# Optimization experiments

Measured on AMD Instinct MI355X. Metric: run time of the kernel, lower is better.

The kernel has to match this reference:

```python
import jax, jax.numpy as jnp
import numpy as np
import math

DIM = 512

def setup_inputs() -> dict:
    key = jax.random.key(0)
    k1, k2, k3, k4 = jax.random.split(key, 4)
    B, SD, SE, D = 32, 512, 512, DIM
    padded_seqs = jax.random.normal(k1, (B, SD, D), dtype=jnp.float32)
    encoder_padded_seqs = jax.random.normal(k2, (B, SE, D), dtype=jnp.float32)
    decoder_mask = jnp.ones((B, SD, 1), dtype=jnp.float32)
    # attention linear: Linear(2*D, D) -> weight (D, 2*D), bias (D,)
    bound = 1.0 / math.sqrt(2 * D)
    W = jax.random.uniform(k3, (D, 2 * D), dtype=jnp.float32, minval=-bound, maxval=bound)
    b = jax.random.uniform(k4, (D,), dtype=jnp.float32, minval=-bound, maxval=bound)
    return {"padded_seqs": padded_seqs, "encoder_padded_seqs": encoder_padded_seqs,
            "decoder_mask": decoder_mask, "W": W, "b": b}

def reference(padded_seqs, encoder_padded_seqs, decoder_mask, W, b):
    D = padded_seqs.shape[-1]
    scale = 1.0 / math.sqrt(D)
    # scores: (B, seq_d, seq_e) via matmul instead of broadcast multiply-sum
    scores = jnp.einsum('bqd,bkd->bqk', padded_seqs, encoder_padded_seqs) * scale
    attention_weights = jax.nn.softmax(scores, axis=2)
    attention_context = jnp.einsum('bqk,bkd->bqd', attention_weights, encoder_padded_seqs)
    cat = jnp.concatenate([padded_seqs, attention_context], axis=2)  # (B, seq_d, 2D)
    attention_masked = jnp.tanh(cat @ W.T + b) * decoder_mask
    return (attention_masked, attention_weights)
```

## Files before the change

### kernel.cpp

```cpp
#include <hip/hip_runtime.h>
#include <math.h>

typedef unsigned short u16;
typedef unsigned int   u32;
typedef __attribute__((ext_vector_type(8))) short bf16x8;
typedef __attribute__((ext_vector_type(4))) float f32x4;

#define BATCH  32
#define SEQ    512
#define DM     512
#define SQE    (SEQ*DM)
#define NBE    ((size_t)BATCH*SQE)

__device__ __forceinline__ u16 f2bf(float x) {
  union { float f; u32 i; } v; v.f = x;
  u32 r = v.i + 0x7fffu + ((v.i >> 16) & 1u);
  return (u16)(r >> 16);
}
__device__ __forceinline__ float fast_tanh(float x) {
  float xc = fminf(fmaxf(x, -15.f), 15.f);
  float e  = __expf(2.f * xc);
  return (e - 1.f) * __builtin_amdgcn_rcpf(e + 1.f);
}

__device__ __forceinline__ void async16(const void* g, void* l) {
  __builtin_amdgcn_global_load_lds(
      (const __attribute__((address_space(1))) void*)g,
      (__attribute__((address_space(3))) void*)l, 16, 0, 0);
}

__device__ __forceinline__ void gemm_bf16(
    const u16* Alo, const u16* Ahi, int ktlo, int kttot, int lda,
    const u16* B, int ldb,
    u16* sA, u16* sB, f32x4 acc[4][4])
{
  const int tid  = threadIdx.x;
  const int lane = tid & 63;
  const int wid  = tid >> 6;
  const int wm = (wid >> 1) * 64;
  const int wn = (wid & 1) * 64;
  const int lm = lane & 15;
  const int lq = lane >> 4;

  const int r0 = tid >> 2, k0 = (tid & 3) * 8;
  u16* lA0 = sA + (size_t)(wid * 64) * 8;
  u16* lA1 = sA + (size_t)(256 + wid * 64) * 8;
  u16* lB0 = sB + (size_t)(wid * 64) * 8;
  u16* lB1 = sB + (size_t)(256 + wid * 64) * 8;

  for (int kt = 0; kt < kttot; ++kt) {
    const u16* Ab = (kt < ktlo) ? (Alo + (size_t)kt * 32)
                                : (Ahi + (size_t)(kt - ktlo) * 32);
    const u16* Bb = B + (size_t)kt * 32;
    async16(Ab + (size_t)r0        * lda + k0, lA0);
    async16(Ab + (size_t)(r0 + 64) * lda + k0, lA1);
    async16(Bb + (size_t)r0        * ldb + k0, lB0);
    async16(Bb + (size_t)(r0 + 64) * ldb + k0, lB1);
    __syncthreads();

    bf16x8 af[4], bv[4];
#pragma unroll
    for (int i = 0; i < 4; ++i) {
      af[i] = *(const bf16x8*)(sA + (wm + i * 16 + lm) * 32 + lq * 8);
      bv[i] = *(const bf16x8*)(sB + (wn + i * 16 + lm) * 32 + lq * 8);
    }
#pragma unroll
    for (int i = 0; i < 4; ++i)
#pragma unroll
      for (int j = 0; j < 4; ++j)
        acc[i][j] = __builtin_amdgcn_mfma_f32_16x16x32_bf16(af[i], bv[j], acc[i][j], 0, 0, 0);
    __syncthreads();
  }
}

__global__ __launch_bounds__(256) void k_prepPW(const float* __restrict__ P,
                                                const float* __restrict__ W,
                                                u16* __restrict__ Pbf,
                                                u16* __restrict__ Wbf)
{
  size_t base = (size_t)blockIdx.x * 2048 + threadIdx.x * 8;
  const float* s; u16* d;
  if (blockIdx.x < 4096) { s = P + base; d = Pbf + base; }
  else { size_t o = base - (size_t)4096 * 2048; s = W + o; d = Wbf + o; }
  float4 a = *(const float4*)s;
  float4 b = *(const float4*)(s + 4);
  bf16x8 v;
  v[0] = (short)f2bf(a.x); v[1] = (short)f2bf(a.y);
  v[2] = (short)f2bf(a.z); v[3] = (short)f2bf(a.w);
  v[4] = (short)f2bf(b.x); v[5] = (short)f2bf(b.y);
  v[6] = (short)f2bf(b.z); v[7] = (short)f2bf(b.w);
  *(bf16x8*)d = v;
}

__global__ __launch_bounds__(256) void k_prepE(const float* __restrict__ E,
                                               u16* __restrict__ Ebf,
                                               u16* __restrict__ EbfT)
{
  __shared__ u16 sT[64][72];
  const int tid = threadIdx.x;
  const int s0 = blockIdx.x * 64, d0 = blockIdx.y * 64, b = blockIdx.z;
  const int r = tid >> 2, c = (tid & 3) * 16;
  const float* src = E + (size_t)b * SQE + (size_t)(s0 + r) * DM + d0 + c;
  float4 x0 = ((const float4*)src)[0];
  float4 x1 = ((const float4*)src)[1];
  float4 x2 = ((const float4*)src)[2];
  float4 x3 = ((const float4*)src)[3];
  float xs[16] = {x0.x,x0.y,x0.z,x0.w, x1.x,x1.y,x1.z,x1.w,
                  x2.x,x2.y,x2.z,x2.w, x3.x,x3.y,x3.z,x3.w};
  u16 v[16];
#pragma unroll
  for (int j = 0; j < 16; ++j) v[j] = f2bf(xs[j]);
  bf16x8 o0, o1;
#pragma unroll
  for (int j = 0; j < 8; ++j) { o0[j] = (short)v[j]; o1[j] = (short)v[8 + j]; }
  u16* dro = Ebf + (size_t)b * SQE + (size_t)(s0 + r) * DM + d0 + c;
  *(bf16x8*)dro = o0;
  *(bf16x8*)(dro + 8) = o1;
#pragma unroll
  for (int j = 0; j < 16; ++j) sT[c + j][r] = v[j];
  __syncthreads();
  const int dr = tid >> 2, sc = (tid & 3) * 16;
  bf16x8 t0, t1;
#pragma unroll
  for (int j = 0; j < 8; ++j) { t0[j] = (short)sT[dr][sc + j]; t1[j] = (short)sT[dr][sc + 8 + j]; }
  u16* dst = EbfT + (size_t)b * SQE + (size_t)(d0 + dr) * SEQ + s0 + sc;
  *(bf16x8*)dst = t0;
  *(bf16x8*)(dst + 8) = t1;
}

__global__ __launch_bounds__(256) void k_scores(const u16* __restrict__ Pbf,
                                                const u16* __restrict__ Ebf,
                                                float* __restrict__ Sc)
{
  __shared__ u16 sA[128 * 32];
  __shared__ u16 sB[128 * 32];
  const int mt = blockIdx.x, nt = blockIdx.y, b = blockIdx.z;
  const u16* A = Pbf + (size_t)b * SQE + (size_t)(mt * 128) * DM;
  const u16* B = Ebf + (size_t)b * SQE + (size_t)(nt * 128) * DM;
  f32x4 acc[4][4] = {};
  gemm_bf16(A, A, 16, 16, DM, B, DM, sA, sB, acc);

  const int tid = threadIdx.x, lane = tid & 63, wid = tid >> 6;
  const int wm = (wid >> 1) * 64, wn = (wid & 1) * 64;
  const int lm = lane & 15, lq = lane >> 4;
  const float scale = 0.044194173824159216f;
  float* out = Sc + (size_t)b * SQE + (size_t)(mt * 128) * SEQ + nt * 128;
#pragma unroll
  for (int i = 0; i < 4; ++i)
#pragma unroll
    for (int j = 0; j < 4; ++j)
#pragma unroll
      for (int r = 0; r < 4; ++r)
        out[(size_t)(wm + i * 16 + lq * 4 + r) * SEQ + wn + j * 16 + lm] = acc[i][j][r] * scale;
}

__global__ __launch_bounds__(256) void v_softmax(const float* __restrict__ Sc,
                                                 float* __restrict__ Wt,
                                                 u16* __restrict__ Wtbf)
{
  const int row  = blockIdx.x * 4 + (threadIdx.x >> 6);
  const int lane = threadIdx.x & 63;
  const float* src = Sc + (size_t)row * SEQ + lane * 8;
  float4 va = ((const float4*)src)[0];
  float4 vb = ((const float4*)src)[1];
  float v[8] = {va.x, va.y, va.z, va.w, vb.x, vb.y, vb.z, vb.w};
  float m = v[0];
#pragma unroll
  for (int j = 1; j < 8; ++j) m = fmaxf(m, v[j]);
#pragma unroll
  for (int off = 32; off > 0; off >>= 1) m = fmaxf(m, __shfl_xor(m, off, 64));
  float s = 0.f;
#pragma unroll
  for (int j = 0; j < 8; ++j) { v[j] = __expf(v[j] - m); s += v[j]; }
#pragma unroll
  for (int off = 32; off > 0; off >>= 1) s += __shfl_xor(s, off, 64);
  const float inv = 1.0f / s;
  float* dst = Wt + (size_t)row * SEQ + lane * 8;
  float4 o0 = {v[0] * inv, v[1] * inv, v[2] * inv, v[3] * inv};
  float4 o1 = {v[4] * inv, v[5] * inv, v[6] * inv, v[7] * inv};
  *(float4*)(dst)     = o0;
  *(float4*)(dst + 4) = o1;
  bf16x8 ob;
#pragma unroll
  for (int j = 0; j < 8; ++j) ob[j] = (short)f2bf(v[j] * inv);
  *(bf16x8*)(Wtbf + (size_t)row * SEQ + lane * 8) = ob;
}

__global__ __launch_bounds__(256) void k_context(const u16* __restrict__ Wtbf,
                                                 const u16* __restrict__ EbfT,
                                                 u16* __restrict__ Ctx)
{
  __shared__ u16 sA[128 * 32];
  __shared__ u16 sB[128 * 32];
  const int mt = blockIdx.x, nt = blockIdx.y, b = blockIdx.z;
  const u16* A = Wtbf + (size_t)b * SQE + (size_t)(mt * 128) * SEQ;
  const u16* B = EbfT + (size_t)b * SQE + (size_t)(nt * 128) * SEQ;
  f32x4 acc[4][4] = {};
  gemm_bf16(A, A, 16, 16, SEQ, B, SEQ, sA, sB, acc);

  const int tid = threadIdx.x, lane = tid & 63, wid = tid >> 6;
  const int wm = (wid >> 1) * 64, wn = (wid & 1) * 64;
  const int lm = lane & 15, lq = lane >> 4;
  u16* out = Ctx + (size_t)b * SQE + (size_t)(mt * 128) * DM + nt * 128;
#pragma unroll
  for (int i = 0; i < 4; ++i)
#pragma unroll
    for (int j = 0; j < 4; ++j)
#pragma unroll
      for (int r = 0; r < 4; ++r)
        out[(size_t)(wm + i * 16 + lq * 4 + r) * DM + wn + j * 16 + lm] = f2bf(acc[i][j][r]);
}

__global__ __launch_bounds__(256) void k_final(const u16* __restrict__ Pbf,
                                               const u16* __restrict__ Ctx,
                                               const u16* __restrict__ Wbf,
                                               const float* __restrict__ bias,
                                               const float* __restrict__ mask,
                                               float* __restrict__ Out)
{
  __shared__ u16 sA[128 * 32];
  __shared__ u16 sB[128 * 32];
  const int mt = blockIdx.x, nt = blockIdx.y, b = blockIdx.z;
  const u16* Alo = Pbf + (size_t)b * SQE + (size_t)(mt * 128) * DM;
  const u16* Ahi = Ctx + (size_t)b * SQE + (size_t)(mt * 128) * DM;
  const u16* B   = Wbf + (size_t)(nt * 128) * 1024;
  f32x4 acc[4][4] = {};
  gemm_bf16(Alo, Ahi, 16, 32, DM, B, 1024, sA, sB, acc);

  const int tid = threadIdx.x, lane = tid & 63, wid = tid >> 6;
  const int wm = (wid >> 1) * 64, wn = (wid & 1) * 64;
  const int lm = lane & 15, lq = lane >> 4;
  float* out = Out + (size_t)b * SQE + (size_t)(mt * 128) * DM + nt * 128;
#pragma unroll
  for (int i = 0; i < 4; ++i)
#pragma unroll
    for (int r = 0; r < 4; ++r) {
      const int row = wm + i * 16 + lq * 4 + r;
      const float mv = mask[b * SEQ + mt * 128 + row];
#pragma unroll
      for (int j = 0; j < 4; ++j) {
        const int col = wn + j * 16 + lm;
        out[(size_t)row * DM + col] = fast_tanh(acc[i][j][r] + bias[nt * 128 + col]) * mv;
      }
    }
}

extern "C" void kernel_launch(void* const* d_in, const int* in_sizes, int n_in,
                              void* d_out, int out_size, void* d_ws, size_t ws_size,
                              hipStream_t stream)
{
  int i8a = -1, i8b = -1, iM = -1, iW = -1, iB = -1;
  for (int i = 0; i < n_in; ++i) {
    const int s = in_sizes[i];
    if (s == BATCH * SQE)      { if (i8a < 0) i8a = i; else i8b = i; }
    else if (s == BATCH * SEQ) iM = i;
    else if (s == DM * 1024)   iW = i;
    else if (s == DM)          iB = i;
  }
  if (i8a < 0) i8a = 0;
  if (i8b < 0) i8b = 1;
  if (iM < 0) iM = 2;
  if (iW < 0) iW = 3;
  if (iB < 0) iB = 4;
  const float* P  = (const float*)d_in[i8a];
  const float* E  = (const float*)d_in[i8b];
  const float* Mk = (const float*)d_in[iM];
  const float* W  = (const float*)d_in[iW];
  const float* Bi = (const float*)d_in[iB];

  float* out0 = (float*)d_out;
  float* out1 = out0 + NBE;

  u16* Pbf  = (u16*)d_ws;
  u16* Ebf  = Pbf  + NBE;
  u16* EbfT = Ebf  + NBE;
  u16* Ctx  = EbfT + NBE;
  u16* Wbf  = Ctx  + NBE;

  dim3 blk(256);
  dim3 gg(4, 4, BATCH);
  k_prepPW <<<dim3(4352), blk, 0, stream>>>(P, W, Pbf, Wbf);
  k_prepE  <<<dim3(8, 8, BATCH), blk, 0, stream>>>(E, Ebf, EbfT);
  k_scores <<<gg, blk, 0, stream>>>(Pbf, Ebf, out0);
  v_softmax<<<dim3(BATCH * SEQ / 4), blk, 0, stream>>>(out0, out1, Ebf );
  k_context<<<gg, blk, 0, stream>>>(Ebf , EbfT, Ctx);
  k_final  <<<gg, blk, 0, stream>>>(Pbf, Ctx, Wbf, Bi, Mk, out0);
}
```

Before: 208.3 us.

## Double-buffer LDS tiles in bf16 GEMM and merge prep kernels into one launch

The shared GEMM loop now uses two LDS buffers. It issues the async global-to-LDS copy for the next K tile before running the MFMAs on the current tile, and it needs one barrier per iteration instead of two. This is meant to hide global load latency behind matrix math in the scores, context and final GEMMs, at the cost of doubling LDS per block. The two conversion kernels (P/W cast and E cast+transpose) are merged into a single launch indexed by block id, removing one kernel launch and its gap.

New measurement: 202.2 us. 2.9% less time.

```diff
diff --git a/kernel.cpp b/kernel.cpp
--- a/kernel.cpp
+++ b/kernel.cpp
@@ -43,26 +43,38 @@
   const int lq = lane >> 4;
 
   const int r0 = tid >> 2, k0 = (tid & 3) * 8;
+  const size_t ao0 = (size_t)r0 * lda + k0;
+  const size_t ao1 = (size_t)(r0 + 64) * lda + k0;
+  const size_t bo0 = (size_t)r0 * ldb + k0;
+  const size_t bo1 = (size_t)(r0 + 64) * ldb + k0;
   u16* lA0 = sA + (size_t)(wid * 64) * 8;
   u16* lA1 = sA + (size_t)(256 + wid * 64) * 8;
   u16* lB0 = sB + (size_t)(wid * 64) * 8;
   u16* lB1 = sB + (size_t)(256 + wid * 64) * 8;
 
+#define STAGE_TILE(kt, h)                                                  \
+  do {                                                                     \
+    const u16* Ab = ((kt) < ktlo) ? (Alo + (size_t)(kt) * 32)              \
+                                  : (Ahi + (size_t)((kt) - ktlo) * 32);    \
+    const u16* Bb = B + (size_t)(kt) * 32;                                 \
+    const int ho = (h) * 4096;                                             \
+    async16(Ab + ao0, lA0 + ho);                                           \
+    async16(Ab + ao1, lA1 + ho);                                           \
+    async16(Bb + bo0, lB0 + ho);                                           \
+    async16(Bb + bo1, lB1 + ho);                                           \
+  } while (0)
+
+  STAGE_TILE(0, 0);
+  __syncthreads();
+  int cur = 0;
   for (int kt = 0; kt < kttot; ++kt) {
-    const u16* Ab = (kt < ktlo) ? (Alo + (size_t)kt * 32)
-                                : (Ahi + (size_t)(kt - ktlo) * 32);
-    const u16* Bb = B + (size_t)kt * 32;
-    async16(Ab + (size_t)r0        * lda + k0, lA0);
-    async16(Ab + (size_t)(r0 + 64) * lda + k0, lA1);
-    async16(Bb + (size_t)r0        * ldb + k0, lB0);
-    async16(Bb + (size_t)(r0 + 64) * ldb + k0, lB1);
-    __syncthreads();
-
+    if (kt + 1 < kttot) STAGE_TILE(kt + 1, cur ^ 1);
+    const int co = cur * 4096;
     bf16x8 af[4], bv[4];
 #pragma unroll
     for (int i = 0; i < 4; ++i) {
-      af[i] = *(const bf16x8*)(sA + (wm + i * 16 + lm) * 32 + lq * 8);
-      bv[i] = *(const bf16x8*)(sB + (wn + i * 16 + lm) * 32 + lq * 8);
+      af[i] = *(const bf16x8*)(sA + co + (wm + i * 16 + lm) * 32 + lq * 8);
+      bv[i] = *(const bf16x8*)(sB + co + (wn + i * 16 + lm) * 32 + lq * 8);
     }
 #pragma unroll
     for (int i = 0; i < 4; ++i)
@@ -70,35 +82,41 @@
       for (int j = 0; j < 4; ++j)
         acc[i][j] = __builtin_amdgcn_mfma_f32_16x16x32_bf16(af[i], bv[j], acc[i][j], 0, 0, 0);
     __syncthreads();
+    cur ^= 1;
   }
-}
-
-__global__ __launch_bounds__(256) void k_prepPW(const float* __restrict__ P,
-                                                const float* __restrict__ W,
-                                                u16* __restrict__ Pbf,
-                                                u16* __restrict__ Wbf)
-{
-  size_t base = (size_t)blockIdx.x * 2048 + threadIdx.x * 8;
-  const float* s; u16* d;
-  if (blockIdx.x < 4096) { s = P + base; d = Pbf + base; }
-  else { size_t o = base - (size_t)4096 * 2048; s = W + o; d = Wbf + o; }
-  float4 a = *(const float4*)s;
-  float4 b = *(const float4*)(s + 4);
-  bf16x8 v;
-  v[0] = (short)f2bf(a.x); v[1] = (short)f2bf(a.y);
-  v[2] = (short)f2bf(a.z); v[3] = (short)f2bf(a.w);
-  v[4] = (short)f2bf(b.x); v[5] = (short)f2bf(b.y);
-  v[6] = (short)f2bf(b.z); v[7] = (short)f2bf(b.w);
-  *(bf16x8*)d = v;
-}
-
-__global__ __launch_bounds__(256) void k_prepE(const float* __restrict__ E,
-                                               u16* __restrict__ Ebf,
-                                               u16* __restrict__ EbfT)
+#undef STAGE_TILE
+}
+
+__global__ __launch_bounds__(256) void k_prep(const float* __restrict__ P,
+                                              const float* __restrict__ W,
+                                              const float* __restrict__ E,
+                                              u16* __restrict__ Pbf,
+                                              u16* __restrict__ Wbf,
+                                              u16* __restrict__ Ebf,
+                                              u16* __restrict__ EbfT)
 {
   __shared__ u16 sT[64][72];
+  const int bx  = blockIdx.x;
   const int tid = threadIdx.x;
-  const int s0 = blockIdx.x * 64, d0 = blockIdx.y * 64, b = blockIdx.z;
+  if (bx < 4352) {
+    size_t base = (size_t)bx * 2048 + tid * 8;
+    const float* s; u16* d;
+    if (bx < 4096) { s = P + base; d = Pbf + base; }
+    else { size_t o = base - (size_t)4096 * 2048; s = W + o; d = Wbf + o; }
+    float4 a = *(const float4*)s;
+    float4 b = *(const float4*)(s + 4);
+    bf16x8 v;
+    v[0] = (short)f2bf(a.x); v[1] = (short)f2bf(a.y);
+    v[2] = (short)f2bf(a.z); v[3] = (short)f2bf(a.w);
+    v[4] = (short)f2bf(b.x); v[5] = (short)f2bf(b.y);
+    v[6] = (short)f2bf(b.z); v[7] = (short)f2bf(b.w);
+    *(bf16x8*)d = v;
+    return;
+  }
+  const int e  = bx - 4352;
+  const int b  = e >> 6;
+  const int s0 = ((e >> 3) & 7) * 64;
+  const int d0 = (e & 7) * 64;
   const int r = tid >> 2, c = (tid & 3) * 16;
   const float* src = E + (size_t)b * SQE + (size_t)(s0 + r) * DM + d0 + c;
   float4 x0 = ((const float4*)src)[0];
@@ -132,8 +150,8 @@
                                                 const u16* __restrict__ Ebf,
                                                 float* __restrict__ Sc)
 {
-  __shared__ u16 sA[128 * 32];
-  __shared__ u16 sB[128 * 32];
+  __shared__ u16 sA[2 * 128 * 32];
+  __shared__ u16 sB[2 * 128 * 32];
   const int mt = blockIdx.x, nt = blockIdx.y, b = blockIdx.z;
   const u16* A = Pbf + (size_t)b * SQE + (size_t)(mt * 128) * DM;
   const u16* B = Ebf + (size_t)b * SQE + (size_t)(nt * 128) * DM;
@@ -190,8 +208,8 @@
                                                  const u16* __restrict__ EbfT,
                                                  u16* __restrict__ Ctx)
 {
-  __shared__ u16 sA[128 * 32];
-  __shared__ u16 sB[128 * 32];
+  __shared__ u16 sA[2 * 128 * 32];
+  __shared__ u16 sB[2 * 128 * 32];
   const int mt = blockIdx.x, nt = blockIdx.y, b = blockIdx.z;
   const u16* A = Wtbf + (size_t)b * SQE + (size_t)(mt * 128) * SEQ;
   const u16* B = EbfT + (size_t)b * SQE + (size_t)(nt * 128) * SEQ;
@@ -218,8 +236,8 @@
                                                const float* __restrict__ mask,
                                                float* __restrict__ Out)
 {
-  __shared__ u16 sA[128 * 32];
-  __shared__ u16 sB[128 * 32];
+  __shared__ u16 sA[2 * 128 * 32];
+  __shared__ u16 sB[2 * 128 * 32];
   const int mt = blockIdx.x, nt = blockIdx.y, b = blockIdx.z;
   const u16* Alo = Pbf + (size_t)b * SQE + (size_t)(mt * 128) * DM;
   const u16* Ahi = Ctx + (size_t)b * SQE + (size_t)(mt * 128) * DM;
@@ -279,8 +297,7 @@
 
   dim3 blk(256);
   dim3 gg(4, 4, BATCH);
-  k_prepPW <<<dim3(4352), blk, 0, stream>>>(P, W, Pbf, Wbf);
-  k_prepE  <<<dim3(8, 8, BATCH), blk, 0, stream>>>(E, Ebf, EbfT);
+  k_prep   <<<dim3(6400), blk, 0, stream>>>(P, W, E, Pbf, Wbf, Ebf, EbfT);
   k_scores <<<gg, blk, 0, stream>>>(Pbf, Ebf, out0);
   v_softmax<<<dim3(BATCH * SEQ / 4), blk, 0, stream>>>(out0, out1, Ebf );
   k_context<<<gg, blk, 0, stream>>>(Ebf , EbfT, Ctx);
```
